# Kernel tuning notes

Hardware: AMD Instinct MI355X
Metric: run time of the kernel (lower is better)

The kernel has to match this reference:

```python
import jax, jax.numpy as jnp
import numpy as np

B, H, S, DK = 2, 16, 2048, 64


def setup_inputs() -> dict:
    key = jax.random.key(0)
    k1, k2, k3, k4 = jax.random.split(key, 4)
    Q = jax.random.normal(k1, (B, H, S, DK), dtype=jnp.float32)
    K = jax.random.normal(k2, (B, H, S, DK), dtype=jnp.float32)
    V = jax.random.normal(k3, (B, H, S, DK), dtype=jnp.float32)
    attn_mask = jax.random.randint(k4, (B, 1, S, S), 0, 2).astype(jnp.bool_)
    return {"Q": Q, "K": K, "V": V, "attn_mask": attn_mask}


def reference(Q, K, V, attn_mask):
    d_k = Q.shape[-1]
    scale = 1.0 / jnp.sqrt(jnp.asarray(d_k, dtype=Q.dtype))
    # scores: [B,H,S,S]
    scores = jnp.einsum('bhqd,bhkd->bhqk', Q, K) * scale
    scores = jnp.where(attn_mask, jnp.asarray(-1e9, dtype=scores.dtype), scores)
    attn = jax.nn.softmax(scores, axis=-1)
    # dropout in eval mode (identity) for deterministic reference
    return jnp.einsum('bhqk,bhkd->bhqd', attn, V)
```

## Files before the change

kernel.cpp:

```cpp
#include <hip/hip_runtime.h>
#include <hip/hip_bf16.h>

#define Bdim 2
#define Hdim 16
#define Sdim 2048
#define Ddim 64
#define KVBLK 64
#define NT (Sdim / KVBLK)
#define WQ 32
#define NWAVE 2
#define QTILE (WQ * NWAVE)
#define QSCL 0.125f
#define SCALE 0.125f

typedef __bf16 bf16x8 __attribute__((ext_vector_type(8)));
typedef float  f32x4  __attribute__((ext_vector_type(4)));
typedef float  f32x16 __attribute__((ext_vector_type(16)));
typedef unsigned u32x4 __attribute__((ext_vector_type(4)));

__device__ __forceinline__ void gll16(const __bf16* g, __bf16* l) {
  __builtin_amdgcn_global_load_lds(
      (const __attribute__((address_space(1))) void*)g,
      (__attribute__((address_space(3))) void*)l, 16, 0, 0);
}
__device__ __forceinline__ unsigned cvtpk_raw(float lo, float hi) {
  unsigned r;
  asm volatile("v_cvt_pk_bf16_f32 %0, %1, %2" : "=v"(r) : "v"(lo), "v"(hi));
  return r;
}
__device__ __forceinline__ unsigned cvtpk(float a, float b, bool sw) {
  const float lo = sw ? b : a;
  const float hi = sw ? a : b;
  return cvtpk_raw(lo, hi);
}

__global__ __launch_bounds__(256) void pack_mask_kernel(
    const void* __restrict__ mask, unsigned long long* __restrict__ packed) {
  const int nwords = Bdim * Sdim * (Sdim / 64);
  const unsigned* m32 = (const unsigned*)mask;
  const unsigned char* m8 = (const unsigned char*)mask;
  int gid = blockIdx.x * blockDim.x + threadIdx.x;
  int lane = gid & 63;
  int wid = gid >> 6;
  int nwaves = (gridDim.x * blockDim.x) >> 6;

  bool isBytes = __any(m32[lane] > 1u);

  for (int w = wid; w < nwords; w += nwaves) {
    int v = isBytes ? (int)m8[(size_t)w * 64 + lane]
                    : (int)m32[(size_t)w * 64 + lane];
    unsigned long long bal = __ballot(v != 0);
    if (lane == 0) packed[w] = bal;
  }
}

__global__ __launch_bounds__(256) void prep_kv(
    const float* __restrict__ K, const float* __restrict__ V,
    __bf16* __restrict__ Kb, __bf16* __restrict__ Vt) {
  __shared__ __bf16 tile[64][72];
  const int bh = blockIdx.y, st = blockIdx.x;
  const int t = threadIdx.x;
  const int r = t >> 2, c0 = (t & 3) << 4;
  {
    const float* ks = K + ((size_t)bh * Sdim + st * 64 + r) * Ddim + c0;
    bf16x8 o0, o1;
#pragma unroll
    for (int j = 0; j < 8; ++j) o0[j] = (__bf16)ks[j];
#pragma unroll
    for (int j = 0; j < 8; ++j) o1[j] = (__bf16)ks[8 + j];
    __bf16* kd = Kb + ((size_t)bh * Sdim + st * 64 + r) * Ddim + c0;
    *(bf16x8*)kd = o0;
    *(bf16x8*)(kd + 8) = o1;
  }
  {
    const float* vs = V + ((size_t)bh * Sdim + st * 64 + r) * Ddim + c0;
#pragma unroll
    for (int j = 0; j < 16; ++j) tile[r][c0 + j] = (__bf16)vs[j];
  }
  __syncthreads();
  {
    const int d = t >> 2, s0 = (t & 3) << 4;
    __bf16 o[16];
#pragma unroll
    for (int j = 0; j < 16; ++j) o[j] = tile[s0 + j][d];
    __bf16* dst = Vt + ((size_t)bh * Ddim + d) * Sdim + st * 64 + s0;
    *(bf16x8*)dst = *(bf16x8*)&o[0];
    *(bf16x8*)(dst + 8) = *(bf16x8*)&o[8];
  }
}

__global__ __launch_bounds__(128, 2) void attn2(
    const float* __restrict__ Q, const __bf16* __restrict__ Kb,
    const __bf16* __restrict__ Vt,
    const unsigned long long* __restrict__ maskP, float* __restrict__ Out) {
  __shared__ alignas(16) __bf16 Kl[2][KVBLK * Ddim];
  __shared__ alignas(16) __bf16 Vl[2][Ddim * KVBLK];

  const int tid = threadIdx.x;
  const int lane = tid & 63;
  const int w = tid >> 6;
  const int l31 = lane & 31;
  const int hi = lane >> 5;
  const int rsw = l31 & 7;

  const int bid = blockIdx.x;
  const int bh = bid & 31;
  const int qt = bid >> 5;
  const int b = bh >> 4;
  const int qrow = qt * QTILE + w * WQ + l31;

  const __bf16* Kbase = Kb + (size_t)bh * Sdim * Ddim;
  const __bf16* Vbase = Vt + (size_t)bh * (size_t)Ddim * Sdim;
  const unsigned long long* mp =
      maskP + ((size_t)b * Sdim + qrow) * (Sdim / 64);

  const bool sw = (cvtpk_raw(0.0f, 1.0f) & 0xFFFFu) != 0u;

  bf16x8 qf[4];
  {
    const float* qs = Q + ((size_t)bh * Sdim + qrow) * Ddim;
#pragma unroll
    for (int step = 0; step < 4; ++step) {
      const int d0 = step * 16 + hi * 8;
      float4 a = *(const float4*)(qs + d0);
      float4 c = *(const float4*)(qs + d0 + 4);
      u32x4 f;
      f[0] = cvtpk(a.x * QSCL, a.y * QSCL, sw);
      f[1] = cvtpk(a.z * QSCL, a.w * QSCL, sw);
      f[2] = cvtpk(c.x * QSCL, c.y * QSCL, sw);
      f[3] = cvtpk(c.z * QSCL, c.w * QSCL, sw);
      qf[step] = __builtin_bit_cast(bf16x8, f);
    }
  }

  const int srow = 32 * w + (lane >> 3);
  const int sblk = (lane & 7) ^ ((lane >> 3) & 7);
  const int dst0 = w * 2048;

#define STAGE(buf, kt_)                                                         \
  do {                                                                          \
    const __bf16* kp_ = Kbase + ((size_t)(kt_)*KVBLK + srow) * Ddim + sblk * 8; \
    gll16(kp_, &Kl[buf][dst0]);                                                 \
    gll16(kp_ + 8 * Ddim, &Kl[buf][dst0 + 512]);                                \
    gll16(kp_ + 16 * Ddim, &Kl[buf][dst0 + 1024]);                              \
    gll16(kp_ + 24 * Ddim, &Kl[buf][dst0 + 1536]);                              \
    const __bf16* vp_ =                                                         \
        Vbase + (size_t)srow * Sdim + (size_t)(kt_)*KVBLK + sblk * 8;           \
    gll16(vp_, &Vl[buf][dst0]);                                                 \
    gll16(vp_ + 8 * Sdim, &Vl[buf][dst0 + 512]);                                \
    gll16(vp_ + 16 * Sdim, &Vl[buf][dst0 + 1024]);                              \
    gll16(vp_ + 24 * Sdim, &Vl[buf][dst0 + 1536]);                              \
  } while (0)

  f32x16 otA = {0,0,0,0,0,0,0,0,0,0,0,0,0,0,0,0};
  f32x16 otB = {0,0,0,0,0,0,0,0,0,0,0,0,0,0,0,0};
  float lrow = 0.f;

  unsigned long long mwCur = mp[0];
  STAGE(0, 0);
  int cur = 0;

#pragma unroll 1
  for (int kt = 0; kt < NT; ++kt) {
    const unsigned long long mwNext = mp[kt + 1 < NT ? kt + 1 : NT - 1];

    if (kt + 1 < NT) {
      STAGE(cur ^ 1, kt + 1);
      asm volatile("s_waitcnt vmcnt(9)" ::: "memory");
    } else {
      asm volatile("s_waitcnt vmcnt(1)" ::: "memory");
    }
    __builtin_amdgcn_s_barrier();
    __builtin_amdgcn_sched_barrier(0);

    f32x16 st0 = {0,0,0,0,0,0,0,0,0,0,0,0,0,0,0,0};
    f32x16 st1 = {0,0,0,0,0,0,0,0,0,0,0,0,0,0,0,0};
    __builtin_amdgcn_s_setprio(1);
#pragma unroll
    for (int step = 0; step < 4; ++step) {
      bf16x8 kf = *(const bf16x8*)&Kl[cur][l31 * 64 + (((step * 2 + hi) ^ rsw) << 3)];
      st0 = __builtin_amdgcn_mfma_f32_32x32x16_bf16(kf, qf[step], st0, 0, 0, 0);
    }
#pragma unroll
    for (int step = 0; step < 4; ++step) {
      bf16x8 kf = *(const bf16x8*)&Kl[cur][(32 + l31) * 64 + (((step * 2 + hi) ^ rsw) << 3)];
      st1 = __builtin_amdgcn_mfma_f32_32x32x16_bf16(kf, qf[step], st1, 0, 0, 0);
    }
    __builtin_amdgcn_s_setprio(0);

    float sv0[16], sv1[16];
    const unsigned w0s = ((unsigned)mwCur) >> (hi * 4);
    const unsigned w1s = ((unsigned)(mwCur >> 32)) >> (hi * 4);
#pragma unroll
    for (int r = 0; r < 16; ++r) {
      const int cr = (r & 3) + 8 * (r >> 2);
      const float e0 = __expf(st0[r]);
      const float e1 = __expf(st1[r]);
      sv0[r] = ((w0s >> cr) & 1u) ? 0.f : e0;
      sv1[r] = ((w1s >> cr) & 1u) ? 0.f : e1;
    }

    float s8[8];
#pragma unroll
    for (int j = 0; j < 8; ++j)
      s8[j] = (sv0[j] + sv0[j + 8]) + (sv1[j] + sv1[j + 8]);
    lrow += ((s8[0] + s8[4]) + (s8[1] + s8[5])) +
            ((s8[2] + s8[6]) + (s8[3] + s8[7]));

    bf16x8 pb[4];
#pragma unroll
    for (int ks = 0; ks < 4; ++ks) {
      const int rb = 8 * (ks & 1);
      unsigned W0, W1, X0, X1;
      if (ks < 2) {
        W0 = cvtpk(sv0[rb + 0], sv0[rb + 1], sw);
        W1 = cvtpk(sv0[rb + 2], sv0[rb + 3], sw);
        X0 = cvtpk(sv0[rb + 4], sv0[rb + 5], sw);
        X1 = cvtpk(sv0[rb + 6], sv0[rb + 7], sw);
      } else {
        W0 = cvtpk(sv1[rb + 0], sv1[rb + 1], sw);
        W1 = cvtpk(sv1[rb + 2], sv1[rb + 3], sw);
        X0 = cvtpk(sv1[rb + 4], sv1[rb + 5], sw);
        X1 = cvtpk(sv1[rb + 6], sv1[rb + 7], sw);
      }
      const unsigned s1 = hi ? W0 : X0;
      const unsigned s2 = hi ? W1 : X1;
      const unsigned r1 = __shfl_xor(s1, 32, 64);
      const unsigned r2 = __shfl_xor(s2, 32, 64);
      u32x4 wv;
      wv[0] = hi ? r1 : W0;
      wv[1] = hi ? r2 : W1;
      wv[2] = hi ? X0 : r1;
      wv[3] = hi ? X1 : r2;
      pb[ks] = __builtin_bit_cast(bf16x8, wv);
    }

    __builtin_amdgcn_s_setprio(1);
#pragma unroll
    for (int ks = 0; ks < 4; ++ks) {
      bf16x8 vf = *(const bf16x8*)&Vl[cur][l31 * 64 + (((ks * 2 + hi) ^ rsw) << 3)];
      otA = __builtin_amdgcn_mfma_f32_32x32x16_bf16(vf, pb[ks], otA, 0, 0, 0);
    }
#pragma unroll
    for (int ks = 0; ks < 4; ++ks) {
      bf16x8 vf = *(const bf16x8*)&Vl[cur][(32 + l31) * 64 + (((ks * 2 + hi) ^ rsw) << 3)];
      otB = __builtin_amdgcn_mfma_f32_32x32x16_bf16(vf, pb[ks], otB, 0, 0, 0);
    }
    __builtin_amdgcn_s_setprio(0);

    mwCur = mwNext;
    __builtin_amdgcn_sched_barrier(0);
    __builtin_amdgcn_s_barrier();
    cur ^= 1;
  }
#undef STAGE

  lrow += __shfl_xor(lrow, 32, 64);
  const float inv = 1.f / (lrow + 1e-30f);
  float* orow = Out + ((size_t)bh * Sdim + qrow) * Ddim;
#pragma unroll
  for (int g = 0; g < 4; ++g) {
    const int d0 = 8 * g + 4 * hi;
    float4 va = {otA[4 * g] * inv, otA[4 * g + 1] * inv,
                 otA[4 * g + 2] * inv, otA[4 * g + 3] * inv};
    float4 vb = {otB[4 * g] * inv, otB[4 * g + 1] * inv,
                 otB[4 * g + 2] * inv, otB[4 * g + 3] * inv};
    *(float4*)(orow + d0) = va;
    *(float4*)(orow + 32 + d0) = vb;
  }
}

__global__ __launch_bounds__(256) void attn_fallback(
    const float* __restrict__ Q, const float* __restrict__ K,
    const float* __restrict__ V, const void* __restrict__ maskRaw,
    float* __restrict__ Out) {
  __shared__ alignas(16) __bf16 Kl[KVBLK * Ddim];
  __shared__ alignas(16) __bf16 Vts[Ddim * KVBLK];
  __shared__ alignas(16) __bf16 Pl[4][16 * 64];

  const int tid = threadIdx.x;
  const int lane = tid & 63;
  const int w = tid >> 6;
  const int lhi = lane >> 4;
  const int llo = lane & 15;

  const int qt = blockIdx.x;
  const int bh = blockIdx.y;
  const int b = bh >> 4;
  const int qbase = qt * 64;

  const float* Qp = Q + (size_t)bh * Sdim * Ddim;
  const float* Kp = K + (size_t)bh * Sdim * Ddim;
  const float* Vp = V + (size_t)bh * Sdim * Ddim;

  bool maskBytes = __any(((const unsigned*)maskRaw)[lane] > 1u);

  bf16x8 qf0, qf1;
  {
    const int qr = qbase + w * 16 + llo;
    const float* src = Qp + (size_t)qr * Ddim + lhi * 8;
#pragma unroll
    for (int i = 0; i < 8; ++i) qf0[i] = (__bf16)(src[i] * SCALE);
#pragma unroll
    for (int i = 0; i < 8; ++i) qf1[i] = (__bf16)(src[32 + i] * SCALE);
  }

  f32x4 acc[4] = {{0.f,0.f,0.f,0.f},{0.f,0.f,0.f,0.f},
                  {0.f,0.f,0.f,0.f},{0.f,0.f,0.f,0.f}};
  float mrow[4], lrw[4];
#pragma unroll
  for (int r = 0; r < 4; ++r) { mrow[r] = -3.0e38f; lrw[r] = 0.f; }

  for (int kt = 0; kt < NT; ++kt) {
    __syncthreads();
    {
      int r = tid >> 2;
      int c0 = (tid & 3) << 4;
      const float* ks = Kp + (size_t)(kt * KVBLK + r) * Ddim + c0;
      const float* vs = Vp + (size_t)(kt * KVBLK + r) * Ddim + c0;
      float kv[16], vv[16];
#pragma unroll
      for (int j = 0; j < 4; ++j) {
        *(float4*)(&kv[j * 4]) = *(const float4*)(ks + j * 4);
        *(float4*)(&vv[j * 4]) = *(const float4*)(vs + j * 4);
      }
      const int swzK = (r & 7) << 3;
      bf16x8 k0v, k1v;
#pragma unroll
      for (int j = 0; j < 8; ++j) { k0v[j] = (__bf16)kv[j]; k1v[j] = (__bf16)kv[8 + j]; }
      *(bf16x8*)&Kl[r * 64 + (c0 ^ swzK)] = k0v;
      *(bf16x8*)&Kl[r * 64 + ((c0 + 8) ^ swzK)] = k1v;
#pragma unroll
      for (int j = 0; j < 16; ++j) {
        int d = c0 + j;
        Vts[d * 64 + (r ^ ((d & 7) << 3))] = (__bf16)vv[j];
      }
    }
    __syncthreads();

    float sv[4][4];
#pragma unroll
    for (int cb = 0; cb < 4; ++cb) {
      int krow = cb * 16 + llo;
      int swz = (krow & 7) << 3;
      bf16x8 kf0 = *(const bf16x8*)&Kl[krow * 64 + ((lhi * 8) ^ swz)];
      bf16x8 kf1 = *(const bf16x8*)&Kl[krow * 64 + ((32 + lhi * 8) ^ swz)];
      f32x4 s = {0.f, 0.f, 0.f, 0.f};
      s = __builtin_amdgcn_mfma_f32_16x16x32_bf16(qf0, kf0, s, 0, 0, 0);
      s = __builtin_amdgcn_mfma_f32_16x16x32_bf16(qf1, kf1, s, 0, 0, 0);
#pragma unroll
      for (int r = 0; r < 4; ++r) {
        size_t q = qbase + w * 16 + lhi * 4 + r;
        size_t k = (size_t)kt * KVBLK + cb * 16 + llo;
        size_t idx = ((size_t)b * Sdim + q) * Sdim + k;
        bool masked = maskBytes ? (((const unsigned char*)maskRaw)[idx] != 0)
                                : (((const int*)maskRaw)[idx] != 0);
        sv[cb][r] = masked ? -1e9f : s[r];
      }
    }

    float corr[4], tsum[4];
#pragma unroll
    for (int r = 0; r < 4; ++r) {
      float mx = fmaxf(fmaxf(sv[0][r], sv[1][r]), fmaxf(sv[2][r], sv[3][r]));
#pragma unroll
      for (int off = 1; off < 16; off <<= 1)
        mx = fmaxf(mx, __shfl_xor(mx, off, 64));
      float mnew = fmaxf(mrow[r], mx);
      corr[r] = __expf(mrow[r] - mnew);
      mrow[r] = mnew;
      tsum[r] = 0.f;
    }
#pragma unroll
    for (int cb = 0; cb < 4; ++cb) {
#pragma unroll
      for (int r = 0; r < 4; ++r) {
        float p = __expf(sv[cb][r] - mrow[r]);
        tsum[r] += p;
        int row = lhi * 4 + r;
        int col = cb * 16 + llo;
        Pl[w][row * 64 + (col ^ ((row & 7) << 3))] = (__bf16)p;
      }
    }
#pragma unroll
    for (int r = 0; r < 4; ++r) {
      float s = tsum[r];
#pragma unroll
      for (int off = 1; off < 16; off <<= 1)
        s += __shfl_xor(s, off, 64);
      lrw[r] = lrw[r] * corr[r] + s;
#pragma unroll
      for (int db = 0; db < 4; ++db) acc[db][r] *= corr[r];
    }
    asm volatile("s_waitcnt lgkmcnt(0)" ::: "memory");

    bf16x8 pf0 = *(const bf16x8*)&Pl[w][llo * 64 + ((lhi * 8) ^ ((llo & 7) << 3))];
    bf16x8 pf1 = *(const bf16x8*)&Pl[w][llo * 64 + ((32 + lhi * 8) ^ ((llo & 7) << 3))];
#pragma unroll
    for (int db = 0; db < 4; ++db) {
      int d = db * 16 + llo;
      int swz = (d & 7) << 3;
      bf16x8 vf0 = *(const bf16x8*)&Vts[d * 64 + ((lhi * 8) ^ swz)];
      bf16x8 vf1 = *(const bf16x8*)&Vts[d * 64 + ((32 + lhi * 8) ^ swz)];
      acc[db] = __builtin_amdgcn_mfma_f32_16x16x32_bf16(pf0, vf0, acc[db], 0, 0, 0);
      acc[db] = __builtin_amdgcn_mfma_f32_16x16x32_bf16(pf1, vf1, acc[db], 0, 0, 0);
    }
  }

#pragma unroll
  for (int r = 0; r < 4; ++r) {
    float inv = 1.f / lrw[r];
    int q = qbase + w * 16 + lhi * 4 + r;
    float* dst = Out + ((size_t)bh * Sdim + q) * Ddim + llo;
#pragma unroll
    for (int db = 0; db < 4; ++db) dst[db * 16] = acc[db][r] * inv;
  }
}

extern "C" void kernel_launch(void* const* d_in, const int* in_sizes, int n_in,
                              void* d_out, int out_size, void* d_ws, size_t ws_size,
                              hipStream_t stream) {
  const float* Q = (const float*)d_in[0];
  const float* K = (const float*)d_in[1];
  const float* V = (const float*)d_in[2];
  const void* mask = d_in[3];
  float* out = (float*)d_out;

  const size_t packed_bytes =
      (size_t)Bdim * Sdim * (Sdim / 64) * sizeof(unsigned long long);
  const size_t tensor_bf16 = (size_t)Bdim * Hdim * Sdim * Ddim * 2;

  if (ws_size >= packed_bytes + 2 * tensor_bf16) {
    unsigned long long* packed = (unsigned long long*)d_ws;
    __bf16* Kb = (__bf16*)((char*)d_ws + packed_bytes);
    __bf16* Vt = (__bf16*)((char*)d_ws + packed_bytes + tensor_bf16);
    pack_mask_kernel<<<512, 256, 0, stream>>>(mask, packed);
    prep_kv<<<dim3(Sdim / 64, Bdim * Hdim), 256, 0, stream>>>(K, V, Kb, Vt);
    attn2<<<(Sdim / QTILE) * Bdim * Hdim, 128, 0, stream>>>(Q, Kb, Vt, packed, out);
  } else {
    attn_fallback<<<dim3(Sdim / 64, Bdim * Hdim), 256, 0, stream>>>(Q, K, V, mask, out);
  }
}
```

Baseline: 108.7 us.

## Use four waves per block with a triple-buffered LDS ring and exp2 softmax

Raises the work-group to four waves (128 query rows per block), which halves the number of blocks and spreads each KV tile's load across more threads. Replaces the double buffer with a three-slot LDS ring, so the second barrier per iteration can be dropped. Folds log2(e) into the Q scale so the exponent becomes a raw exp2. Splits the bf16 packing into templated branches on the swap flag. The main risks are a race in the ring and fewer blocks per CU (24KB...48KB LDS, 256 threads), which could lower occupancy or parallelism across the 1024→512 blocks.

```diff
diff --git a/kernel.cpp b/kernel.cpp
--- a/kernel.cpp
+++ b/kernel.cpp
@@ -8,10 +8,12 @@
 #define KVBLK 64
 #define NT (Sdim / KVBLK)
 #define WQ 32
-#define NWAVE 2
+#define NWAVE 4
 #define QTILE (WQ * NWAVE)
-#define QSCL 0.125f
+#define QSCL (0.125f * 1.44269504088896f)
 #define SCALE 0.125f
+#define BUFE 8192
+#define VOFF 4096
 
 typedef __bf16 bf16x8 __attribute__((ext_vector_type(8)));
 typedef float  f32x4  __attribute__((ext_vector_type(4)));
@@ -25,13 +27,37 @@
 }
 __device__ __forceinline__ unsigned cvtpk_raw(float lo, float hi) {
   unsigned r;
-  asm volatile("v_cvt_pk_bf16_f32 %0, %1, %2" : "=v"(r) : "v"(lo), "v"(hi));
+  asm("v_cvt_pk_bf16_f32 %0, %1, %2" : "=v"(r) : "v"(lo), "v"(hi));
   return r;
+}
+template <bool SW>
+__device__ __forceinline__ unsigned pko(float a, float b) {
+  return SW ? cvtpk_raw(b, a) : cvtpk_raw(a, b);
 }
 __device__ __forceinline__ unsigned cvtpk(float a, float b, bool sw) {
   const float lo = sw ? b : a;
   const float hi = sw ? a : b;
   return cvtpk_raw(lo, hi);
+}
+template <bool SW>
+__device__ __forceinline__ void packAll(const float (&sv0)[16],
+                                        const float (&sv1)[16],
+                                        unsigned (&pw)[16]) {
+#pragma unroll
+  for (int ks = 0; ks < 4; ++ks) {
+    const int rb = 8 * (ks & 1);
+    if (ks < 2) {
+      pw[ks * 4 + 0] = pko<SW>(sv0[rb + 0], sv0[rb + 1]);
+      pw[ks * 4 + 1] = pko<SW>(sv0[rb + 2], sv0[rb + 3]);
+      pw[ks * 4 + 2] = pko<SW>(sv0[rb + 4], sv0[rb + 5]);
+      pw[ks * 4 + 3] = pko<SW>(sv0[rb + 6], sv0[rb + 7]);
+    } else {
+      pw[ks * 4 + 0] = pko<SW>(sv1[rb + 0], sv1[rb + 1]);
+      pw[ks * 4 + 1] = pko<SW>(sv1[rb + 2], sv1[rb + 3]);
+      pw[ks * 4 + 2] = pko<SW>(sv1[rb + 4], sv1[rb + 5]);
+      pw[ks * 4 + 3] = pko<SW>(sv1[rb + 6], sv1[rb + 7]);
+    }
+  }
 }
 
 __global__ __launch_bounds__(256) void pack_mask_kernel(
@@ -89,12 +115,11 @@
   }
 }
 
-__global__ __launch_bounds__(128, 2) void attn2(
+__global__ __launch_bounds__(256, 2) void attn4(
     const float* __restrict__ Q, const __bf16* __restrict__ Kb,
     const __bf16* __restrict__ Vt,
     const unsigned long long* __restrict__ maskP, float* __restrict__ Out) {
-  __shared__ alignas(16) __bf16 Kl[2][KVBLK * Ddim];
-  __shared__ alignas(16) __bf16 Vl[2][Ddim * KVBLK];
+  __shared__ alignas(16) __bf16 sm[3 * BUFE];
 
   const int tid = threadIdx.x;
   const int lane = tid & 63;
@@ -133,23 +158,19 @@
     }
   }
 
-  const int srow = 32 * w + (lane >> 3);
+  const int srow = 16 * w + (lane >> 3);
   const int sblk = (lane & 7) ^ ((lane >> 3) & 7);
-  const int dst0 = w * 2048;
-
-#define STAGE(buf, kt_)                                                         \
+  const int dstw = w * 1024;
+
+#define STAGE(off_, kt_)                                                        \
   do {                                                                          \
     const __bf16* kp_ = Kbase + ((size_t)(kt_)*KVBLK + srow) * Ddim + sblk * 8; \
-    gll16(kp_, &Kl[buf][dst0]);                                                 \
-    gll16(kp_ + 8 * Ddim, &Kl[buf][dst0 + 512]);                                \
-    gll16(kp_ + 16 * Ddim, &Kl[buf][dst0 + 1024]);                              \
-    gll16(kp_ + 24 * Ddim, &Kl[buf][dst0 + 1536]);                              \
+    gll16(kp_, &sm[(off_) + dstw]);                                             \
+    gll16(kp_ + 8 * Ddim, &sm[(off_) + dstw + 512]);                            \
     const __bf16* vp_ =                                                         \
         Vbase + (size_t)srow * Sdim + (size_t)(kt_)*KVBLK + sblk * 8;           \
-    gll16(vp_, &Vl[buf][dst0]);                                                 \
-    gll16(vp_ + 8 * Sdim, &Vl[buf][dst0 + 512]);                                \
-    gll16(vp_ + 16 * Sdim, &Vl[buf][dst0 + 1024]);                              \
-    gll16(vp_ + 24 * Sdim, &Vl[buf][dst0 + 1536]);                              \
+    gll16(vp_, &sm[(off_) + VOFF + dstw]);                                      \
+    gll16(vp_ + 8 * Sdim, &sm[(off_) + VOFF + dstw + 512]);                     \
   } while (0)
 
   f32x16 otA = {0,0,0,0,0,0,0,0,0,0,0,0,0,0,0,0};
@@ -158,15 +179,14 @@
 
   unsigned long long mwCur = mp[0];
   STAGE(0, 0);
-  int cur = 0;
+  int rdOff = 0, stOff = BUFE;
 
 #pragma unroll 1
   for (int kt = 0; kt < NT; ++kt) {
     const unsigned long long mwNext = mp[kt + 1 < NT ? kt + 1 : NT - 1];
-
     if (kt + 1 < NT) {
-      STAGE(cur ^ 1, kt + 1);
-      asm volatile("s_waitcnt vmcnt(9)" ::: "memory");
+      STAGE(stOff, kt + 1);
+      asm volatile("s_waitcnt vmcnt(5)" ::: "memory");
     } else {
       asm volatile("s_waitcnt vmcnt(1)" ::: "memory");
     }
@@ -178,12 +198,12 @@
     __builtin_amdgcn_s_setprio(1);
 #pragma unroll
     for (int step = 0; step < 4; ++step) {
-      bf16x8 kf = *(const bf16x8*)&Kl[cur][l31 * 64 + (((step * 2 + hi) ^ rsw) << 3)];
+      bf16x8 kf = *(const bf16x8*)&sm[rdOff + l31 * 64 + (((step * 2 + hi) ^ rsw) << 3)];
       st0 = __builtin_amdgcn_mfma_f32_32x32x16_bf16(kf, qf[step], st0, 0, 0, 0);
     }
 #pragma unroll
     for (int step = 0; step < 4; ++step) {
-      bf16x8 kf = *(const bf16x8*)&Kl[cur][(32 + l31) * 64 + (((step * 2 + hi) ^ rsw) << 3)];
+      bf16x8 kf = *(const bf16x8*)&sm[rdOff + (32 + l31) * 64 + (((step * 2 + hi) ^ rsw) << 3)];
       st1 = __builtin_amdgcn_mfma_f32_32x32x16_bf16(kf, qf[step], st1, 0, 0, 0);
     }
     __builtin_amdgcn_s_setprio(0);
@@ -194,8 +214,8 @@
 #pragma unroll
     for (int r = 0; r < 16; ++r) {
       const int cr = (r & 3) + 8 * (r >> 2);
-      const float e0 = __expf(st0[r]);
-      const float e1 = __expf(st1[r]);
+      const float e0 = __builtin_amdgcn_exp2f(st0[r]);
+      const float e1 = __builtin_amdgcn_exp2f(st1[r]);
       sv0[r] = ((w0s >> cr) & 1u) ? 0.f : e0;
       sv1[r] = ((w1s >> cr) & 1u) ? 0.f : e1;
     }
@@ -207,22 +227,14 @@
     lrow += ((s8[0] + s8[4]) + (s8[1] + s8[5])) +
             ((s8[2] + s8[6]) + (s8[3] + s8[7]));
 
+    unsigned pw[16];
+    if (!sw) packAll<false>(sv0, sv1, pw);
+    else     packAll<true>(sv0, sv1, pw);
     bf16x8 pb[4];
 #pragma unroll
     for (int ks = 0; ks < 4; ++ks) {
-      const int rb = 8 * (ks & 1);
-      unsigned W0, W1, X0, X1;
-      if (ks < 2) {
-        W0 = cvtpk(sv0[rb + 0], sv0[rb + 1], sw);
-        W1 = cvtpk(sv0[rb + 2], sv0[rb + 3], sw);
-        X0 = cvtpk(sv0[rb + 4], sv0[rb + 5], sw);
-        X1 = cvtpk(sv0[rb + 6], sv0[rb + 7], sw);
-      } else {
-        W0 = cvtpk(sv1[rb + 0], sv1[rb + 1], sw);
-        W1 = cvtpk(sv1[rb + 2], sv1[rb + 3], sw);
-        X0 = cvtpk(sv1[rb + 4], sv1[rb + 5], sw);
-        X1 = cvtpk(sv1[rb + 6], sv1[rb + 7], sw);
-      }
+      const unsigned W0 = pw[ks * 4 + 0], W1 = pw[ks * 4 + 1];
+      const unsigned X0 = pw[ks * 4 + 2], X1 = pw[ks * 4 + 3];
       const unsigned s1 = hi ? W0 : X0;
       const unsigned s2 = hi ? W1 : X1;
       const unsigned r1 = __shfl_xor(s1, 32, 64);
@@ -238,20 +250,19 @@
     __builtin_amdgcn_s_setprio(1);
 #pragma unroll
     for (int ks = 0; ks < 4; ++ks) {
-      bf16x8 vf = *(const bf16x8*)&Vl[cur][l31 * 64 + (((ks * 2 + hi) ^ rsw) << 3)];
+      bf16x8 vf = *(const bf16x8*)&sm[rdOff + VOFF + l31 * 64 + (((ks * 2 + hi) ^ rsw) << 3)];
       otA = __builtin_amdgcn_mfma_f32_32x32x16_bf16(vf, pb[ks], otA, 0, 0, 0);
     }
 #pragma unroll
     for (int ks = 0; ks < 4; ++ks) {
-      bf16x8 vf = *(const bf16x8*)&Vl[cur][(32 + l31) * 64 + (((ks * 2 + hi) ^ rsw) << 3)];
+      bf16x8 vf = *(const bf16x8*)&sm[rdOff + VOFF + (32 + l31) * 64 + (((ks * 2 + hi) ^ rsw) << 3)];
       otB = __builtin_amdgcn_mfma_f32_32x32x16_bf16(vf, pb[ks], otB, 0, 0, 0);
     }
     __builtin_amdgcn_s_setprio(0);
 
     mwCur = mwNext;
-    __builtin_amdgcn_sched_barrier(0);
-    __builtin_amdgcn_s_barrier();
-    cur ^= 1;
+    rdOff = stOff;
+    stOff = (stOff == 2 * BUFE) ? 0 : stOff + BUFE;
   }
 #undef STAGE
 
@@ -436,7 +447,7 @@
     __bf16* Vt = (__bf16*)((char*)d_ws + packed_bytes + tensor_bf16);
     pack_mask_kernel<<<512, 256, 0, stream>>>(mask, packed);
     prep_kv<<<dim3(Sdim / 64, Bdim * Hdim), 256, 0, stream>>>(K, V, Kb, Vt);
-    attn2<<<(Sdim / QTILE) * Bdim * Hdim, 128, 0, stream>>>(Q, Kb, Vt, packed, out);
+    attn4<<<(Sdim / QTILE) * Bdim * Hdim, 256, 0, stream>>>(Q, Kb, Vt, packed, out);
   } else {
     attn_fallback<<<dim3(Sdim / 64, Bdim * Hdim), 256, 0, stream>>>(Q, K, V, mask, out);
   }
```

Result: faster. 95.41 us (-12.2%).
